# Optimization experiments

Hardware: AMD Instinct MI355X
Metric: run time of the kernel (lower is better)

## Reference

```python
import jax, jax.numpy as jnp
import numpy as np

MIN_DURATION = 0.0
MAX_DURATION = 75.0
MAX_LEN = 80  # hard-coded output length from regulate_length's slice/pad to 80
LN_EPS = 1e-6


def _conv1d_same(x, w, b):
    # x: [B, T, Cin], w: [K, Cin, Cout] -> [B, T, Cout]
    y = jax.lax.conv_general_dilated(
        x, w, window_strides=(1,), padding='SAME',
        dimension_numbers=('NWC', 'WIO', 'NWC'))
    return y + b


def _layernorm(x, gamma, beta):
    mu = jnp.mean(x, axis=-1, keepdims=True)
    var = jnp.mean(jnp.square(x - mu), axis=-1, keepdims=True)
    return (x - mu) * jax.lax.rsqrt(var + LN_EPS) * gamma + beta


def setup_inputs() -> dict:
    key = jax.random.key(0)
    ks = jax.random.split(key, 5)
    B, T, D, F, K = 2048, 128, 256, 256, 3
    scale = 0.05
    return {
        'encoder_output': jax.random.normal(ks[0], (B, T, D), jnp.float32),
        'conv1_w': jax.random.normal(ks[1], (K, D, F), jnp.float32) * scale,
        'conv1_b': jnp.zeros((F,), jnp.float32),
        'conv2_w': jax.random.normal(ks[2], (K, F, F), jnp.float32) * scale,
        'conv2_b': jnp.zeros((F,), jnp.float32),
        'ln_gamma': jnp.ones((F,), jnp.float32),
        'ln_beta': jnp.zeros((F,), jnp.float32),
        'dense_w': jax.random.normal(ks[3], (F, 1), jnp.float32) * scale,
        'dense_b': jnp.full((1,), 2.0, jnp.float32),  # bias so rounded durations are nontrivial
    }


def reference(encoder_output, conv1_w, conv1_b, conv2_w, conv2_b,
              ln_gamma, ln_beta, dense_w, dense_b):
    # --- variance predictor (dropout = identity at inference) ---
    x = jax.nn.relu(_conv1d_same(encoder_output, conv1_w, conv1_b))
    x = _layernorm(x, ln_gamma, ln_beta)
    x = jax.nn.relu(_conv1d_same(x, conv2_w, conv2_b))
    x = _layernorm(x, ln_gamma, ln_beta)
    predicted_durations = x @ dense_w + dense_b  # [B, T, 1]

    # --- regulate_length, fully vectorized over batch ---
    dur = jnp.round(jnp.clip(predicted_durations, MIN_DURATION, MAX_DURATION))
    dur = dur[..., 0].astype(jnp.int32)                 # [B, T]
    cum = jnp.cumsum(dur, axis=1)                       # [B, T]
    pos = jnp.arange(MAX_LEN, dtype=jnp.int32)          # [80]
    # source index for each output frame: searchsorted(cum, pos, side='right')
    idx = jnp.sum(pos[None, :, None] >= cum[:, None, :], axis=-1)  # [B, 80]
    valid = pos[None, :] < cum[:, -1:]                  # [B, 80]
    T = encoder_output.shape[1]
    gathered = jnp.take_along_axis(
        encoder_output, jnp.clip(idx, 0, T - 1)[..., None], axis=1)  # [B, 80, D]
    regulated = jnp.where(valid[..., None], gathered, 0.0)
    return regulated
```

## Files before the change

### kernel.cpp

```cpp
#include <hip/hip_runtime.h>
#include <hip/hip_bf16.h>
#include <math.h>

#define TT 128
#define CC 256
#define MAXLEN 80
#define KSTEPS 24
#define SLOTS 68
#define NCH16 32

typedef __attribute__((ext_vector_type(8))) _Float16 half8v;
typedef __attribute__((ext_vector_type(2))) _Float16 half2v;
typedef __attribute__((ext_vector_type(4))) float f32x4;

#define MSCALE 4096.0f
#define MINV   (1.0f/4096.0f)

__device__ __forceinline__ int chunkidx(int slot, int c16) {
    return slot * NCH16 + (c16 ^ (slot & 7));
}

__device__ __forceinline__ void split2(float x0, float x1, half2v& h, half2v& m) {
    h = __builtin_bit_cast(half2v, __builtin_amdgcn_cvt_pkrtz(x0, x1));
    m.x = (_Float16)fmaf((float)h.x, -MSCALE, x0 * MSCALE);
    m.y = (_Float16)fmaf((float)h.y, -MSCALE, x1 * MSCALE);
}

__global__ void va_prep(const float* __restrict__ w1, const float* __restrict__ w2,
                        half8v* __restrict__ wsB)
{
    const int idx = blockIdx.x * 256 + threadIdx.x;
    const int lane = idx & 63;
    int q = idx >> 6;
    const int nfg = q & 15;   q >>= 4;
    const int plane = q & 1;  q >>= 1;
    const int kk2 = q & 7;    q >>= 3;
    const int tap = q % 3;
    const int cv  = q / 3;
    const float* w = cv ? w2 : w1;
    const int co  = nfg * 16 + (lane & 15);
    const int ci0 = kk2 * 32 + (lane >> 4) * 8;
    half8v out;
    #pragma unroll
    for (int j = 0; j < 8; ++j) {
        const float x = w[tap * (CC * CC) + (ci0 + j) * CC + co];
        const _Float16 h = (_Float16)x;
        if (plane == 0) out[j] = h;
        else            out[j] = (_Float16)((x - (float)h) * MSCALE);
    }
    wsB[idx] = out;
}

__global__ __launch_bounds__(256, 2)
void va_c1(const float* __restrict__ enc,
           const float* __restrict__ b1g,
           const float* __restrict__ gg,  const float* __restrict__ bbg,
           const half8v* __restrict__ wsB,
           half8v* __restrict__ x1G)
{
    __shared__ half8v P[2][SLOTS * NCH16];
    __shared__ float sumS[4][64];
    __shared__ float sumQ[4][64];
    __shared__ float muS[64];
    __shared__ float rsS[64];

    const int bb   = blockIdx.x;
    const int b    = bb >> 1;
    const int base = (bb & 1) << 6;
    const int tid  = threadIdx.x;
    const int wid  = tid >> 6;
    const int lane = tid & 63;
    const int l15  = lane & 15;
    const int lg   = lane >> 4;
    const int NGc  = wid * 64;

    const f32x4* encB4 = reinterpret_cast<const f32x4*>(enc) + (size_t)b * (TT * 64);

    for (int m2 = tid; m2 < SLOTS * NCH16; m2 += 256) {
        const int slot = m2 >> 5;
        const int c16  = m2 & 31;
        const int ra   = base + slot - 2;
        half8v h8, m8;
        if (ra >= 0 && ra < TT) {
            const f32x4* src = encB4 + ra * 64 + c16 * 2;
            const f32x4 v0 = src[0], v1 = src[1];
            half2v hp, mp;
            split2(v0.x, v0.y, hp, mp); h8[0]=hp.x; h8[1]=hp.y; m8[0]=mp.x; m8[1]=mp.y;
            split2(v0.z, v0.w, hp, mp); h8[2]=hp.x; h8[3]=hp.y; m8[2]=mp.x; m8[3]=mp.y;
            split2(v1.x, v1.y, hp, mp); h8[4]=hp.x; h8[5]=hp.y; m8[4]=mp.x; m8[5]=mp.y;
            split2(v1.z, v1.w, hp, mp); h8[6]=hp.x; h8[7]=hp.y; m8[6]=mp.x; m8[7]=mp.y;
        } else {
            #pragma unroll
            for (int j = 0; j < 8; ++j) { h8[j] = (_Float16)0.f; m8[j] = (_Float16)0.f; }
        }
        const int ci = chunkidx(slot, c16);
        P[0][ci] = h8;
        P[1][ci] = m8;
    }
    __syncthreads();

    float gv[4], bvv[4];
    #pragma unroll
    for (int nf = 0; nf < 4; ++nf) {
        gv[nf]  = gg[NGc + nf * 16 + l15];
        bvv[nf] = bbg[NGc + nf * 16 + l15];
    }

    f32x4 accH[4][4];
    f32x4 accM[4][4];
    #pragma unroll
    for (int nf = 0; nf < 4; ++nf) {
        const float bz = b1g[NGc + nf * 16 + l15];
        const f32x4 b4 = {bz, bz, bz, bz};
        const f32x4 z4 = {0.f, 0.f, 0.f, 0.f};
        #pragma unroll
        for (int mf = 0; mf < 4; ++mf) { accH[mf][nf] = b4; accM[mf][nf] = z4; }
    }

    half8v B0[8], B1[8];
    auto loadB = [&](half8v (&Bp)[8], int ks) {
        const int tap = ks >> 3, kk2 = ks & 7;
        const int fb = (tap * 8 + kk2) * 2;
        #pragma unroll
        for (int p = 0; p < 2; ++p)
            #pragma unroll
            for (int nf = 0; nf < 4; ++nf)
                Bp[p * 4 + nf] = wsB[(size_t)((fb + p) * 16 + (wid * 4 + nf)) * 64 + lane];
    };
    auto doK = [&](const half8v (&Bp)[8], int ks) {
        const int tap = ks >> 3, kk2 = ks & 7;
        #pragma unroll
        for (int mf = 0; mf < 4; ++mf) {
            const int slot = mf * 16 + l15 + tap + 1;
            const int ci = chunkidx(slot, kk2 * 4 + lg);
            const half8v Ah = P[0][ci];
            const half8v Am = P[1][ci];
            #pragma unroll
            for (int nf = 0; nf < 4; ++nf) {
                accH[mf][nf] = __builtin_amdgcn_mfma_f32_16x16x32_f16(Ah, Bp[nf],     accH[mf][nf], 0, 0, 0);
                accM[mf][nf] = __builtin_amdgcn_mfma_f32_16x16x32_f16(Ah, Bp[4 + nf], accM[mf][nf], 0, 0, 0);
                accM[mf][nf] = __builtin_amdgcn_mfma_f32_16x16x32_f16(Am, Bp[nf],     accM[mf][nf], 0, 0, 0);
            }
        }
    };
    loadB(B0, 0);
    #pragma unroll 1
    for (int ks = 0; ks < KSTEPS; ks += 2) {
        loadB(B1, ks + 1);
        doK(B0, ks);
        if (ks + 2 < KSTEPS) loadB(B0, ks + 2);
        doK(B1, ks + 1);
    }

    #pragma unroll
    for (int mf = 0; mf < 4; ++mf)
        #pragma unroll
        for (int nf = 0; nf < 4; ++nf) {
            f32x4 v;
            #pragma unroll
            for (int e = 0; e < 4; ++e)
                v[e] = fmaxf(fmaf(accM[mf][nf][e], MINV, accH[mf][nf][e]), 0.f);
            accH[mf][nf] = v;
        }

    #pragma unroll
    for (int mf = 0; mf < 4; ++mf)
        #pragma unroll
        for (int r = 0; r < 4; ++r) {
            float s = (accH[mf][0][r] + accH[mf][1][r]) + (accH[mf][2][r] + accH[mf][3][r]);
            float q = accH[mf][0][r] * accH[mf][0][r];
            q = fmaf(accH[mf][1][r], accH[mf][1][r], q);
            q = fmaf(accH[mf][2][r], accH[mf][2][r], q);
            q = fmaf(accH[mf][3][r], accH[mf][3][r], q);
            #pragma unroll
            for (int o = 1; o < 16; o <<= 1) {
                s += __shfl_xor(s, o, 64);
                q += __shfl_xor(q, o, 64);
            }
            if (l15 == 0) {
                const int idx = mf * 16 + lg * 4 + r;
                sumS[wid][idx] = s;
                sumQ[wid][idx] = q;
            }
        }
    __syncthreads();
    {
        const int i = lane;
        const float S = (sumS[0][i] + sumS[1][i]) + (sumS[2][i] + sumS[3][i]);
        const float Q = (sumQ[0][i] + sumQ[1][i]) + (sumQ[2][i] + sumQ[3][i]);
        const float mu = S * (1.f / 256.f);
        const float var = fmaf(-mu, mu, Q * (1.f / 256.f));
        muS[i] = mu;
        rsS[i] = 1.0f / sqrtf(var + 1e-6f);
    }
    _Float16* Ph = (_Float16*)&P[0][0];
    _Float16* Pm = (_Float16*)&P[1][0];
    #pragma unroll
    for (int mf = 0; mf < 4; ++mf)
        #pragma unroll
        for (int r = 0; r < 4; ++r) {
            const int row = mf * 16 + lg * 4 + r;
            const float mu = muS[row];
            const float rs = rsS[row];
            #pragma unroll
            for (int nf = 0; nf < 4; ++nf) {
                const float v = (accH[mf][nf][r] - mu) * rs * gv[nf] + bvv[nf];
                const int col = NGc + nf * 16 + l15;
                const int off = chunkidx(row + 2, col >> 3) * 8 + (col & 7);
                const _Float16 h = (_Float16)v;
                Ph[off] = h;
                Pm[off] = (_Float16)fmaf((float)h, -MSCALE, v * MSCALE);
            }
        }
    __syncthreads();

    for (int g = tid; g < 2 * 64 * NCH16; g += 256) {
        const int plane = g >> 11;
        const int rem   = g & 2047;
        const int rl    = rem >> 5;
        const int c     = rem & 31;
        x1G[((size_t)(b * 2 + plane) * TT + base + rl) * NCH16 + c] =
            P[plane][(rl + 2) * NCH16 + c];
    }
}

__global__ __launch_bounds__(256, 2)
void va_c2(const half8v* __restrict__ x1G,
           const float* __restrict__ b2g,
           const float* __restrict__ gg,  const float* __restrict__ bbg,
           const float* __restrict__ dwg, const float* __restrict__ dbg,
           const half8v* __restrict__ wsB,
           int* __restrict__ durG)
{
    __shared__ half8v P[2][SLOTS * NCH16];
    __shared__ float sumS[4][64];
    __shared__ float sumQ[4][64];
    __shared__ float muS[64];
    __shared__ float rsS[64];
    __shared__ float dsum[4][64];

    const int bb   = blockIdx.x;
    const int b    = bb >> 1;
    const int base = (bb & 1) << 6;
    const int tid  = threadIdx.x;
    const int wid  = tid >> 6;
    const int lane = tid & 63;
    const int l15  = lane & 15;
    const int lg   = lane >> 4;
    const int NGc  = wid * 64;

    half8v* Plin = &P[0][0];
    for (int g = tid; g < 2 * SLOTS * NCH16; g += 256) {
        const int plane = (g < SLOTS * NCH16) ? 0 : 1;
        const int rem   = g - plane * (SLOTS * NCH16);
        const int slot  = rem >> 5;
        const int c     = rem & 31;
        const int row   = base + slot - 2;
        half8v v;
        if (row >= 0 && row < TT) {
            v = x1G[((size_t)(b * 2 + plane) * TT + row) * NCH16 + c];
        } else {
            #pragma unroll
            for (int j = 0; j < 8; ++j) v[j] = (_Float16)0.f;
        }
        Plin[g] = v;
    }
    __syncthreads();

    float gv[4], bvv[4], dv[4];
    #pragma unroll
    for (int nf = 0; nf < 4; ++nf) {
        gv[nf]  = gg[NGc + nf * 16 + l15];
        bvv[nf] = bbg[NGc + nf * 16 + l15];
        dv[nf]  = dwg[NGc + nf * 16 + l15];
    }

    f32x4 accH[4][4];
    f32x4 accM[4][4];
    #pragma unroll
    for (int nf = 0; nf < 4; ++nf) {
        const float bz = b2g[NGc + nf * 16 + l15];
        const f32x4 b4 = {bz, bz, bz, bz};
        const f32x4 z4 = {0.f, 0.f, 0.f, 0.f};
        #pragma unroll
        for (int mf = 0; mf < 4; ++mf) { accH[mf][nf] = b4; accM[mf][nf] = z4; }
    }

    half8v B0[8], B1[8];
    auto loadB = [&](half8v (&Bp)[8], int ks) {
        const int tap = ks >> 3, kk2 = ks & 7;
        const int fb = ((3 + tap) * 8 + kk2) * 2;
        #pragma unroll
        for (int p = 0; p < 2; ++p)
            #pragma unroll
            for (int nf = 0; nf < 4; ++nf)
                Bp[p * 4 + nf] = wsB[(size_t)((fb + p) * 16 + (wid * 4 + nf)) * 64 + lane];
    };
    auto doK = [&](const half8v (&Bp)[8], int ks) {
        const int tap = ks >> 3, kk2 = ks & 7;
        #pragma unroll
        for (int mf = 0; mf < 4; ++mf) {
            const int slot = mf * 16 + l15 + tap + 1;
            const int ci = chunkidx(slot, kk2 * 4 + lg);
            const half8v Ah = P[0][ci];
            const half8v Am = P[1][ci];
            #pragma unroll
            for (int nf = 0; nf < 4; ++nf) {
                accH[mf][nf] = __builtin_amdgcn_mfma_f32_16x16x32_f16(Ah, Bp[nf],     accH[mf][nf], 0, 0, 0);
                accM[mf][nf] = __builtin_amdgcn_mfma_f32_16x16x32_f16(Ah, Bp[4 + nf], accM[mf][nf], 0, 0, 0);
                accM[mf][nf] = __builtin_amdgcn_mfma_f32_16x16x32_f16(Am, Bp[nf],     accM[mf][nf], 0, 0, 0);
            }
        }
    };
    loadB(B0, 0);
    #pragma unroll 1
    for (int ks = 0; ks < KSTEPS; ks += 2) {
        loadB(B1, ks + 1);
        doK(B0, ks);
        if (ks + 2 < KSTEPS) loadB(B0, ks + 2);
        doK(B1, ks + 1);
    }

    #pragma unroll
    for (int mf = 0; mf < 4; ++mf)
        #pragma unroll
        for (int nf = 0; nf < 4; ++nf) {
            f32x4 v;
            #pragma unroll
            for (int e = 0; e < 4; ++e)
                v[e] = fmaxf(fmaf(accM[mf][nf][e], MINV, accH[mf][nf][e]), 0.f);
            accH[mf][nf] = v;
        }

    #pragma unroll
    for (int mf = 0; mf < 4; ++mf)
        #pragma unroll
        for (int r = 0; r < 4; ++r) {
            float s = (accH[mf][0][r] + accH[mf][1][r]) + (accH[mf][2][r] + accH[mf][3][r]);
            float q = accH[mf][0][r] * accH[mf][0][r];
            q = fmaf(accH[mf][1][r], accH[mf][1][r], q);
            q = fmaf(accH[mf][2][r], accH[mf][2][r], q);
            q = fmaf(accH[mf][3][r], accH[mf][3][r], q);
            #pragma unroll
            for (int o = 1; o < 16; o <<= 1) {
                s += __shfl_xor(s, o, 64);
                q += __shfl_xor(q, o, 64);
            }
            if (l15 == 0) {
                const int idx = mf * 16 + lg * 4 + r;
                sumS[wid][idx] = s;
                sumQ[wid][idx] = q;
            }
        }
    __syncthreads();
    {
        const int i = lane;
        const float S = (sumS[0][i] + sumS[1][i]) + (sumS[2][i] + sumS[3][i]);
        const float Q = (sumQ[0][i] + sumQ[1][i]) + (sumQ[2][i] + sumQ[3][i]);
        const float mu = S * (1.f / 256.f);
        const float var = fmaf(-mu, mu, Q * (1.f / 256.f));
        muS[i] = mu;
        rsS[i] = 1.0f / sqrtf(var + 1e-6f);
    }
    #pragma unroll
    for (int mf = 0; mf < 4; ++mf)
        #pragma unroll
        for (int r = 0; r < 4; ++r) {
            const int row = mf * 16 + lg * 4 + r;
            const float mu = muS[row];
            const float rs = rsS[row];
            float p = 0.f;
            #pragma unroll
            for (int nf = 0; nf < 4; ++nf) {
                const float v = (accH[mf][nf][r] - mu) * rs * gv[nf] + bvv[nf];
                p = fmaf(v, dv[nf], p);
            }
            #pragma unroll
            for (int o = 1; o < 16; o <<= 1) p += __shfl_xor(p, o, 64);
            if (l15 == 0) dsum[wid][row] = p;
        }
    __syncthreads();
    if (tid < 64) {
        const float pd = (dsum[0][tid] + dsum[1][tid]) + (dsum[2][tid] + dsum[3][tid]) + dbg[0];
        const float dcl = fminf(fmaxf(pd, 0.0f), 75.0f);
        durG[b * TT + base + tid] = (int)rintf(dcl);
    }
}

__global__ __launch_bounds__(256)
void va_gather(const float* __restrict__ enc, const int* __restrict__ durG,
               float* __restrict__ outg)
{
    __shared__ int cumS[TT];
    __shared__ int wtotS[2];
    const int b    = blockIdx.x;
    const int tid  = threadIdx.x;
    const int wid  = tid >> 6;
    const int lane = tid & 63;

    int sv = 0;
    if (tid < TT) {
        sv = durG[b * TT + tid];
        #pragma unroll
        for (int o = 1; o < 64; o <<= 1) {
            const int u = __shfl_up(sv, o, 64);
            if (lane >= o) sv += u;
        }
        if (lane == 63) wtotS[tid >> 6] = sv;
    }
    __syncthreads();
    if (tid < TT) {
        if (tid >= 64) sv += wtotS[0];
        cumS[tid] = sv;
    }
    __syncthreads();

    const int total = cumS[TT - 1];
    const f32x4* encB4 = reinterpret_cast<const f32x4*>(enc) + (size_t)b * (TT * 64);
    f32x4* outB4 = reinterpret_cast<f32x4*>(outg) + (size_t)b * (MAXLEN * 64);
    for (int pp = 0; pp < 20; ++pp) {
        const int p = wid * 20 + pp;
        int lo = 0, hi = TT;
        while (lo < hi) {
            const int mid = (lo + hi) >> 1;
            if (cumS[mid] <= p) lo = mid + 1; else hi = mid;
        }
        f32x4 v = {0.f, 0.f, 0.f, 0.f};
        if (p < total) {
            const int src = (lo < TT) ? lo : (TT - 1);
            v = encB4[src * 64 + lane];
        }
        outB4[p * 64 + lane] = v;
    }
}

extern "C" void kernel_launch(void* const* d_in, const int* in_sizes, int n_in,
                              void* d_out, int out_size, void* d_ws, size_t ws_size,
                              hipStream_t stream) {
    const float* enc = (const float*)d_in[0];
    const float* w1  = (const float*)d_in[1];
    const float* b1  = (const float*)d_in[2];
    const float* w2  = (const float*)d_in[3];
    const float* b2  = (const float*)d_in[4];
    const float* gam = (const float*)d_in[5];
    const float* bet = (const float*)d_in[6];
    const float* dw  = (const float*)d_in[7];
    const float* db  = (const float*)d_in[8];
    float* out = (float*)d_out;

    const int B = in_sizes[0] / (TT * CC);
    char* wp = (char*)d_ws;
    half8v* wsB = (half8v*)wp;               wp += 98304u * 16u;
    int* durG   = (int*)wp;                  wp += (size_t)B * TT * 4;
    half8v* x1G = (half8v*)wp;

    const size_t used = (size_t)(wp - (char*)d_ws);
    const size_t perBatch = (size_t)2 * TT * NCH16 * 16;
    size_t avail = (ws_size > used) ? (ws_size - used) : 0;
    int chunkB = (int)(avail / perBatch);
    if (chunkB < 1) chunkB = 1;
    if (chunkB > B) chunkB = B;

    hipLaunchKernelGGL(va_prep, dim3(384), dim3(256), 0, stream, w1, w2, wsB);
    for (int b0 = 0; b0 < B; b0 += chunkB) {
        const int nb = (b0 + chunkB <= B) ? chunkB : (B - b0);
        hipLaunchKernelGGL(va_c1, dim3(nb * 2), dim3(256), 0, stream,
                           enc + (size_t)b0 * TT * CC, b1, gam, bet, wsB, x1G);
        hipLaunchKernelGGL(va_c2, dim3(nb * 2), dim3(256), 0, stream,
                           x1G, b2, gam, bet, dw, db, wsB, durG + (size_t)b0 * TT);
    }
    hipLaunchKernelGGL(va_gather, dim3(B), dim3(256), 0, stream, enc, durG, out);
}
```

Before: 674.3 us.

## Switch conv GEMMs to 32x32x16 MFMA tiles and batch global loads before LDS staging

Both conv kernels now use 32x32x16 f16 MFMA instead of 16x16x32. The prepacked weight layout, accumulator layout, LayerNorm row indexing and shuffle reductions are all rewritten to match. The larger tile is meant to cut LDS A-fragment reads and instruction count per FLOP. Global loads for LDS staging are issued all at once into registers before conversion, to raise memory-level parallelism. Nontemporal loads and stores are added for streaming data. This costs more registers per thread and risks lower occupancy.

```diff
diff --git a/kernel.cpp b/kernel.cpp
--- a/kernel.cpp
+++ b/kernel.cpp
@@ -5,13 +5,14 @@
 #define TT 128
 #define CC 256
 #define MAXLEN 80
-#define KSTEPS 24
+#define KS2 48
 #define SLOTS 68
 #define NCH16 32
 
-typedef __attribute__((ext_vector_type(8))) _Float16 half8v;
-typedef __attribute__((ext_vector_type(2))) _Float16 half2v;
-typedef __attribute__((ext_vector_type(4))) float f32x4;
+typedef __attribute__((ext_vector_type(8)))  _Float16 half8v;
+typedef __attribute__((ext_vector_type(2)))  _Float16 half2v;
+typedef __attribute__((ext_vector_type(4)))  float    f32x4;
+typedef __attribute__((ext_vector_type(16))) float    f32x16;
 
 #define MSCALE 4096.0f
 #define MINV   (1.0f/4096.0f)
@@ -32,14 +33,14 @@
     const int idx = blockIdx.x * 256 + threadIdx.x;
     const int lane = idx & 63;
     int q = idx >> 6;
-    const int nfg = q & 15;   q >>= 4;
+    const int nfg = q & 7;    q >>= 3;
     const int plane = q & 1;  q >>= 1;
-    const int kk2 = q & 7;    q >>= 3;
+    const int kk = q & 15;    q >>= 4;
     const int tap = q % 3;
     const int cv  = q / 3;
     const float* w = cv ? w2 : w1;
-    const int co  = nfg * 16 + (lane & 15);
-    const int ci0 = kk2 * 32 + (lane >> 4) * 8;
+    const int co  = nfg * 32 + (lane & 31);
+    const int ci0 = kk * 16 + (lane >> 5) * 8;
     half8v out;
     #pragma unroll
     for (int j = 0; j < 8; ++j) {
@@ -70,115 +71,126 @@
     const int tid  = threadIdx.x;
     const int wid  = tid >> 6;
     const int lane = tid & 63;
-    const int l15  = lane & 15;
-    const int lg   = lane >> 4;
+    const int l31  = lane & 31;
+    const int hi   = lane >> 5;
     const int NGc  = wid * 64;
 
     const f32x4* encB4 = reinterpret_cast<const f32x4*>(enc) + (size_t)b * (TT * 64);
 
-    for (int m2 = tid; m2 < SLOTS * NCH16; m2 += 256) {
-        const int slot = m2 >> 5;
-        const int c16  = m2 & 31;
-        const int ra   = base + slot - 2;
-        half8v h8, m8;
-        if (ra >= 0 && ra < TT) {
-            const f32x4* src = encB4 + ra * 64 + c16 * 2;
-            const f32x4 v0 = src[0], v1 = src[1];
-            half2v hp, mp;
-            split2(v0.x, v0.y, hp, mp); h8[0]=hp.x; h8[1]=hp.y; m8[0]=mp.x; m8[1]=mp.y;
-            split2(v0.z, v0.w, hp, mp); h8[2]=hp.x; h8[3]=hp.y; m8[2]=mp.x; m8[3]=mp.y;
-            split2(v1.x, v1.y, hp, mp); h8[4]=hp.x; h8[5]=hp.y; m8[4]=mp.x; m8[5]=mp.y;
-            split2(v1.z, v1.w, hp, mp); h8[6]=hp.x; h8[7]=hp.y; m8[6]=mp.x; m8[7]=mp.y;
-        } else {
-            #pragma unroll
-            for (int j = 0; j < 8; ++j) { h8[j] = (_Float16)0.f; m8[j] = (_Float16)0.f; }
-        }
-        const int ci = chunkidx(slot, c16);
-        P[0][ci] = h8;
-        P[1][ci] = m8;
-    }
-    __syncthreads();
-
-    float gv[4], bvv[4];
-    #pragma unroll
-    for (int nf = 0; nf < 4; ++nf) {
-        gv[nf]  = gg[NGc + nf * 16 + l15];
-        bvv[nf] = bbg[NGc + nf * 16 + l15];
-    }
-
-    f32x4 accH[4][4];
-    f32x4 accM[4][4];
-    #pragma unroll
-    for (int nf = 0; nf < 4; ++nf) {
-        const float bz = b1g[NGc + nf * 16 + l15];
-        const f32x4 b4 = {bz, bz, bz, bz};
-        const f32x4 z4 = {0.f, 0.f, 0.f, 0.f};
-        #pragma unroll
-        for (int mf = 0; mf < 4; ++mf) { accH[mf][nf] = b4; accM[mf][nf] = z4; }
-    }
-
-    half8v B0[8], B1[8];
-    auto loadB = [&](half8v (&Bp)[8], int ks) {
-        const int tap = ks >> 3, kk2 = ks & 7;
-        const int fb = (tap * 8 + kk2) * 2;
+    {
+        f32x4 sa[9], sb[9];
+        #pragma unroll
+        for (int it = 0; it < 9; ++it) {
+            const f32x4 z = {0.f, 0.f, 0.f, 0.f};
+            sa[it] = z; sb[it] = z;
+            const int m2 = tid + it * 256;
+            if (m2 < SLOTS * NCH16) {
+                const int slot = m2 >> 5;
+                const int c16  = m2 & 31;
+                const int ra   = base + slot - 2;
+                if (ra >= 0 && ra < TT) {
+                    const f32x4* src = encB4 + ra * 64 + c16 * 2;
+                    sa[it] = __builtin_nontemporal_load(src);
+                    sb[it] = __builtin_nontemporal_load(src + 1);
+                }
+            }
+        }
+        #pragma unroll
+        for (int it = 0; it < 9; ++it) {
+            const int m2 = tid + it * 256;
+            if (m2 < SLOTS * NCH16) {
+                const f32x4 v0 = sa[it], v1 = sb[it];
+                half8v h8, m8;
+                half2v hp, mp;
+                split2(v0.x, v0.y, hp, mp); h8[0]=hp.x; h8[1]=hp.y; m8[0]=mp.x; m8[1]=mp.y;
+                split2(v0.z, v0.w, hp, mp); h8[2]=hp.x; h8[3]=hp.y; m8[2]=mp.x; m8[3]=mp.y;
+                split2(v1.x, v1.y, hp, mp); h8[4]=hp.x; h8[5]=hp.y; m8[4]=mp.x; m8[5]=mp.y;
+                split2(v1.z, v1.w, hp, mp); h8[6]=hp.x; h8[7]=hp.y; m8[6]=mp.x; m8[7]=mp.y;
+                const int ci = chunkidx(m2 >> 5, m2 & 31);
+                P[0][ci] = h8;
+                P[1][ci] = m8;
+            }
+        }
+    }
+    __syncthreads();
+
+    float gv[2], bvv[2];
+    #pragma unroll
+    for (int nf = 0; nf < 2; ++nf) {
+        gv[nf]  = gg[NGc + nf * 32 + l31];
+        bvv[nf] = bbg[NGc + nf * 32 + l31];
+    }
+
+    f32x16 accH[2][2];
+    f32x16 accM[2][2];
+    #pragma unroll
+    for (int nf = 0; nf < 2; ++nf) {
+        const float bz = b1g[NGc + nf * 32 + l31];
+        #pragma unroll
+        for (int mf = 0; mf < 2; ++mf)
+            #pragma unroll
+            for (int e = 0; e < 16; ++e) { accH[mf][nf][e] = bz; accM[mf][nf][e] = 0.f; }
+    }
+
+    half8v B0[4], B1[4];
+    auto loadB = [&](half8v (&Bp)[4], int ks) {
+        const int tap = ks >> 4, kk = ks & 15;
+        const int fb = ((0 * 3 + tap) * 16 + kk) * 2;
         #pragma unroll
         for (int p = 0; p < 2; ++p)
             #pragma unroll
-            for (int nf = 0; nf < 4; ++nf)
-                Bp[p * 4 + nf] = wsB[(size_t)((fb + p) * 16 + (wid * 4 + nf)) * 64 + lane];
+            for (int nf = 0; nf < 2; ++nf)
+                Bp[p * 2 + nf] = wsB[(size_t)((fb + p) * 8 + (wid * 2 + nf)) * 64 + lane];
     };
-    auto doK = [&](const half8v (&Bp)[8], int ks) {
-        const int tap = ks >> 3, kk2 = ks & 7;
-        #pragma unroll
-        for (int mf = 0; mf < 4; ++mf) {
-            const int slot = mf * 16 + l15 + tap + 1;
-            const int ci = chunkidx(slot, kk2 * 4 + lg);
+    auto doK = [&](const half8v (&Bp)[4], int ks) {
+        const int tap = ks >> 4, kk = ks & 15;
+        #pragma unroll
+        for (int mf = 0; mf < 2; ++mf) {
+            const int slot = mf * 32 + l31 + tap + 1;
+            const int ci = chunkidx(slot, kk * 2 + hi);
             const half8v Ah = P[0][ci];
             const half8v Am = P[1][ci];
             #pragma unroll
-            for (int nf = 0; nf < 4; ++nf) {
-                accH[mf][nf] = __builtin_amdgcn_mfma_f32_16x16x32_f16(Ah, Bp[nf],     accH[mf][nf], 0, 0, 0);
-                accM[mf][nf] = __builtin_amdgcn_mfma_f32_16x16x32_f16(Ah, Bp[4 + nf], accM[mf][nf], 0, 0, 0);
-                accM[mf][nf] = __builtin_amdgcn_mfma_f32_16x16x32_f16(Am, Bp[nf],     accM[mf][nf], 0, 0, 0);
-            }
+            for (int nf = 0; nf < 2; ++nf)
+                accH[mf][nf] = __builtin_amdgcn_mfma_f32_32x32x16_f16(Ah, Bp[nf],     accH[mf][nf], 0, 0, 0);
+            #pragma unroll
+            for (int nf = 0; nf < 2; ++nf)
+                accM[mf][nf] = __builtin_amdgcn_mfma_f32_32x32x16_f16(Ah, Bp[2 + nf], accM[mf][nf], 0, 0, 0);
+            #pragma unroll
+            for (int nf = 0; nf < 2; ++nf)
+                accM[mf][nf] = __builtin_amdgcn_mfma_f32_32x32x16_f16(Am, Bp[nf],     accM[mf][nf], 0, 0, 0);
         }
     };
     loadB(B0, 0);
     #pragma unroll 1
-    for (int ks = 0; ks < KSTEPS; ks += 2) {
+    for (int ks = 0; ks < KS2; ks += 2) {
         loadB(B1, ks + 1);
         doK(B0, ks);
-        if (ks + 2 < KSTEPS) loadB(B0, ks + 2);
+        if (ks + 2 < KS2) loadB(B0, ks + 2);
         doK(B1, ks + 1);
     }
 
     #pragma unroll
-    for (int mf = 0; mf < 4; ++mf)
-        #pragma unroll
-        for (int nf = 0; nf < 4; ++nf) {
-            f32x4 v;
-            #pragma unroll
-            for (int e = 0; e < 4; ++e)
-                v[e] = fmaxf(fmaf(accM[mf][nf][e], MINV, accH[mf][nf][e]), 0.f);
-            accH[mf][nf] = v;
-        }
-
-    #pragma unroll
-    for (int mf = 0; mf < 4; ++mf)
-        #pragma unroll
-        for (int r = 0; r < 4; ++r) {
-            float s = (accH[mf][0][r] + accH[mf][1][r]) + (accH[mf][2][r] + accH[mf][3][r]);
-            float q = accH[mf][0][r] * accH[mf][0][r];
-            q = fmaf(accH[mf][1][r], accH[mf][1][r], q);
-            q = fmaf(accH[mf][2][r], accH[mf][2][r], q);
-            q = fmaf(accH[mf][3][r], accH[mf][3][r], q);
-            #pragma unroll
-            for (int o = 1; o < 16; o <<= 1) {
+    for (int mf = 0; mf < 2; ++mf)
+        #pragma unroll
+        for (int nf = 0; nf < 2; ++nf)
+            #pragma unroll
+            for (int e = 0; e < 16; ++e)
+                accH[mf][nf][e] = fmaxf(fmaf(accM[mf][nf][e], MINV, accH[mf][nf][e]), 0.f);
+
+    #pragma unroll
+    for (int mf = 0; mf < 2; ++mf)
+        #pragma unroll
+        for (int r = 0; r < 16; ++r) {
+            float s = accH[mf][0][r] + accH[mf][1][r];
+            float q = fmaf(accH[mf][0][r], accH[mf][0][r], accH[mf][1][r] * accH[mf][1][r]);
+            #pragma unroll
+            for (int o = 1; o < 32; o <<= 1) {
                 s += __shfl_xor(s, o, 64);
                 q += __shfl_xor(q, o, 64);
             }
-            if (l15 == 0) {
-                const int idx = mf * 16 + lg * 4 + r;
+            if (l31 == 0) {
+                const int idx = mf * 32 + (r & 3) + 8 * (r >> 2) + 4 * hi;
                 sumS[wid][idx] = s;
                 sumQ[wid][idx] = q;
             }
@@ -196,16 +208,16 @@
     _Float16* Ph = (_Float16*)&P[0][0];
     _Float16* Pm = (_Float16*)&P[1][0];
     #pragma unroll
-    for (int mf = 0; mf < 4; ++mf)
-        #pragma unroll
-        for (int r = 0; r < 4; ++r) {
-            const int row = mf * 16 + lg * 4 + r;
+    for (int mf = 0; mf < 2; ++mf)
+        #pragma unroll
+        for (int r = 0; r < 16; ++r) {
+            const int row = mf * 32 + (r & 3) + 8 * (r >> 2) + 4 * hi;
             const float mu = muS[row];
             const float rs = rsS[row];
             #pragma unroll
-            for (int nf = 0; nf < 4; ++nf) {
+            for (int nf = 0; nf < 2; ++nf) {
                 const float v = (accH[mf][nf][r] - mu) * rs * gv[nf] + bvv[nf];
-                const int col = NGc + nf * 16 + l15;
+                const int col = NGc + nf * 32 + l31;
                 const int off = chunkidx(row + 2, col >> 3) * 8 + (col & 7);
                 const _Float16 h = (_Float16)v;
                 Ph[off] = h;
@@ -245,109 +257,112 @@
     const int tid  = threadIdx.x;
     const int wid  = tid >> 6;
     const int lane = tid & 63;
-    const int l15  = lane & 15;
-    const int lg   = lane >> 4;
+    const int l31  = lane & 31;
+    const int hi   = lane >> 5;
     const int NGc  = wid * 64;
 
-    half8v* Plin = &P[0][0];
-    for (int g = tid; g < 2 * SLOTS * NCH16; g += 256) {
-        const int plane = (g < SLOTS * NCH16) ? 0 : 1;
-        const int rem   = g - plane * (SLOTS * NCH16);
-        const int slot  = rem >> 5;
-        const int c     = rem & 31;
-        const int row   = base + slot - 2;
-        half8v v;
-        if (row >= 0 && row < TT) {
-            v = x1G[((size_t)(b * 2 + plane) * TT + row) * NCH16 + c];
-        } else {
-            #pragma unroll
-            for (int j = 0; j < 8; ++j) v[j] = (_Float16)0.f;
-        }
-        Plin[g] = v;
-    }
-    __syncthreads();
-
-    float gv[4], bvv[4], dv[4];
-    #pragma unroll
-    for (int nf = 0; nf < 4; ++nf) {
-        gv[nf]  = gg[NGc + nf * 16 + l15];
-        bvv[nf] = bbg[NGc + nf * 16 + l15];
-        dv[nf]  = dwg[NGc + nf * 16 + l15];
-    }
-
-    f32x4 accH[4][4];
-    f32x4 accM[4][4];
-    #pragma unroll
-    for (int nf = 0; nf < 4; ++nf) {
-        const float bz = b2g[NGc + nf * 16 + l15];
-        const f32x4 b4 = {bz, bz, bz, bz};
-        const f32x4 z4 = {0.f, 0.f, 0.f, 0.f};
-        #pragma unroll
-        for (int mf = 0; mf < 4; ++mf) { accH[mf][nf] = b4; accM[mf][nf] = z4; }
-    }
-
-    half8v B0[8], B1[8];
-    auto loadB = [&](half8v (&Bp)[8], int ks) {
-        const int tap = ks >> 3, kk2 = ks & 7;
-        const int fb = ((3 + tap) * 8 + kk2) * 2;
+    {
+        half8v sx[17];
+        #pragma unroll
+        for (int it = 0; it < 17; ++it) {
+            const int g = tid + it * 256;
+            const int plane = (g >= SLOTS * NCH16) ? 1 : 0;
+            const int rem   = g - plane * (SLOTS * NCH16);
+            const int slot  = rem >> 5;
+            const int c     = rem & 31;
+            const int row   = base + slot - 2;
+            if (row >= 0 && row < TT) {
+                sx[it] = x1G[((size_t)(b * 2 + plane) * TT + row) * NCH16 + c];
+            } else {
+                #pragma unroll
+                for (int j = 0; j < 8; ++j) sx[it][j] = (_Float16)0.f;
+            }
+        }
+        half8v* Plin = &P[0][0];
+        #pragma unroll
+        for (int it = 0; it < 17; ++it)
+            Plin[tid + it * 256] = sx[it];
+    }
+    __syncthreads();
+
+    float gv[2], bvv[2], dv[2];
+    #pragma unroll
+    for (int nf = 0; nf < 2; ++nf) {
+        gv[nf]  = gg[NGc + nf * 32 + l31];
+        bvv[nf] = bbg[NGc + nf * 32 + l31];
+        dv[nf]  = dwg[NGc + nf * 32 + l31];
+    }
+
+    f32x16 accH[2][2];
+    f32x16 accM[2][2];
+    #pragma unroll
+    for (int nf = 0; nf < 2; ++nf) {
+        const float bz = b2g[NGc + nf * 32 + l31];
+        #pragma unroll
+        for (int mf = 0; mf < 2; ++mf)
+            #pragma unroll
+            for (int e = 0; e < 16; ++e) { accH[mf][nf][e] = bz; accM[mf][nf][e] = 0.f; }
+    }
+
+    half8v B0[4], B1[4];
+    auto loadB = [&](half8v (&Bp)[4], int ks) {
+        const int tap = ks >> 4, kk = ks & 15;
+        const int fb = ((1 * 3 + tap) * 16 + kk) * 2;
         #pragma unroll
         for (int p = 0; p < 2; ++p)
             #pragma unroll
-            for (int nf = 0; nf < 4; ++nf)
-                Bp[p * 4 + nf] = wsB[(size_t)((fb + p) * 16 + (wid * 4 + nf)) * 64 + lane];
+            for (int nf = 0; nf < 2; ++nf)
+                Bp[p * 2 + nf] = wsB[(size_t)((fb + p) * 8 + (wid * 2 + nf)) * 64 + lane];
     };
-    auto doK = [&](const half8v (&Bp)[8], int ks) {
-        const int tap = ks >> 3, kk2 = ks & 7;
-        #pragma unroll
-        for (int mf = 0; mf < 4; ++mf) {
-            const int slot = mf * 16 + l15 + tap + 1;
-            const int ci = chunkidx(slot, kk2 * 4 + lg);
+    auto doK = [&](const half8v (&Bp)[4], int ks) {
+        const int tap = ks >> 4, kk = ks & 15;
+        #pragma unroll
+        for (int mf = 0; mf < 2; ++mf) {
+            const int slot = mf * 32 + l31 + tap + 1;
+            const int ci = chunkidx(slot, kk * 2 + hi);
             const half8v Ah = P[0][ci];
             const half8v Am = P[1][ci];
             #pragma unroll
-            for (int nf = 0; nf < 4; ++nf) {
-                accH[mf][nf] = __builtin_amdgcn_mfma_f32_16x16x32_f16(Ah, Bp[nf],     accH[mf][nf], 0, 0, 0);
-                accM[mf][nf] = __builtin_amdgcn_mfma_f32_16x16x32_f16(Ah, Bp[4 + nf], accM[mf][nf], 0, 0, 0);
-                accM[mf][nf] = __builtin_amdgcn_mfma_f32_16x16x32_f16(Am, Bp[nf],     accM[mf][nf], 0, 0, 0);
-            }
+            for (int nf = 0; nf < 2; ++nf)
+                accH[mf][nf] = __builtin_amdgcn_mfma_f32_32x32x16_f16(Ah, Bp[nf],     accH[mf][nf], 0, 0, 0);
+            #pragma unroll
+            for (int nf = 0; nf < 2; ++nf)
+                accM[mf][nf] = __builtin_amdgcn_mfma_f32_32x32x16_f16(Ah, Bp[2 + nf], accM[mf][nf], 0, 0, 0);
+            #pragma unroll
+            for (int nf = 0; nf < 2; ++nf)
+                accM[mf][nf] = __builtin_amdgcn_mfma_f32_32x32x16_f16(Am, Bp[nf],     accM[mf][nf], 0, 0, 0);
         }
     };
     loadB(B0, 0);
     #pragma unroll 1
-    for (int ks = 0; ks < KSTEPS; ks += 2) {
+    for (int ks = 0; ks < KS2; ks += 2) {
         loadB(B1, ks + 1);
         doK(B0, ks);
-        if (ks + 2 < KSTEPS) loadB(B0, ks + 2);
+        if (ks + 2 < KS2) loadB(B0, ks + 2);
         doK(B1, ks + 1);
     }
 
     #pragma unroll
-    for (int mf = 0; mf < 4; ++mf)
-        #pragma unroll
-        for (int nf = 0; nf < 4; ++nf) {
-            f32x4 v;
-            #pragma unroll
-            for (int e = 0; e < 4; ++e)
-                v[e] = fmaxf(fmaf(accM[mf][nf][e], MINV, accH[mf][nf][e]), 0.f);
-            accH[mf][nf] = v;
-        }
-
-    #pragma unroll
-    for (int mf = 0; mf < 4; ++mf)
-        #pragma unroll
-        for (int r = 0; r < 4; ++r) {
-            float s = (accH[mf][0][r] + accH[mf][1][r]) + (accH[mf][2][r] + accH[mf][3][r]);
-            float q = accH[mf][0][r] * accH[mf][0][r];
-            q = fmaf(accH[mf][1][r], accH[mf][1][r], q);
-            q = fmaf(accH[mf][2][r], accH[mf][2][r], q);
-            q = fmaf(accH[mf][3][r], accH[mf][3][r], q);
-            #pragma unroll
-            for (int o = 1; o < 16; o <<= 1) {
+    for (int mf = 0; mf < 2; ++mf)
+        #pragma unroll
+        for (int nf = 0; nf < 2; ++nf)
+            #pragma unroll
+            for (int e = 0; e < 16; ++e)
+                accH[mf][nf][e] = fmaxf(fmaf(accM[mf][nf][e], MINV, accH[mf][nf][e]), 0.f);
+
+    #pragma unroll
+    for (int mf = 0; mf < 2; ++mf)
+        #pragma unroll
+        for (int r = 0; r < 16; ++r) {
+            float s = accH[mf][0][r] + accH[mf][1][r];
+            float q = fmaf(accH[mf][0][r], accH[mf][0][r], accH[mf][1][r] * accH[mf][1][r]);
+            #pragma unroll
+            for (int o = 1; o < 32; o <<= 1) {
                 s += __shfl_xor(s, o, 64);
                 q += __shfl_xor(q, o, 64);
             }
-            if (l15 == 0) {
-                const int idx = mf * 16 + lg * 4 + r;
+            if (l31 == 0) {
+                const int idx = mf * 32 + (r & 3) + 8 * (r >> 2) + 4 * hi;
                 sumS[wid][idx] = s;
                 sumQ[wid][idx] = q;
             }
@@ -363,21 +378,21 @@
         rsS[i] = 1.0f / sqrtf(var + 1e-6f);
     }
     #pragma unroll
-    for (int mf = 0; mf < 4; ++mf)
-        #pragma unroll
-        for (int r = 0; r < 4; ++r) {
-            const int row = mf * 16 + lg * 4 + r;
+    for (int mf = 0; mf < 2; ++mf)
+        #pragma unroll
+        for (int r = 0; r < 16; ++r) {
+            const int row = mf * 32 + (r & 3) + 8 * (r >> 2) + 4 * hi;
             const float mu = muS[row];
             const float rs = rsS[row];
             float p = 0.f;
             #pragma unroll
-            for (int nf = 0; nf < 4; ++nf) {
+            for (int nf = 0; nf < 2; ++nf) {
                 const float v = (accH[mf][nf][r] - mu) * rs * gv[nf] + bvv[nf];
                 p = fmaf(v, dv[nf], p);
             }
             #pragma unroll
-            for (int o = 1; o < 16; o <<= 1) p += __shfl_xor(p, o, 64);
-            if (l15 == 0) dsum[wid][row] = p;
+            for (int o = 1; o < 32; o <<= 1) p += __shfl_xor(p, o, 64);
+            if (l31 == 0) dsum[wid][row] = p;
         }
     __syncthreads();
     if (tid < 64) {
@@ -420,17 +435,17 @@
     f32x4* outB4 = reinterpret_cast<f32x4*>(outg) + (size_t)b * (MAXLEN * 64);
     for (int pp = 0; pp < 20; ++pp) {
         const int p = wid * 20 + pp;
-        int lo = 0, hi = TT;
-        while (lo < hi) {
-            const int mid = (lo + hi) >> 1;
-            if (cumS[mid] <= p) lo = mid + 1; else hi = mid;
+        int lo = 0, hi2 = TT;
+        while (lo < hi2) {
+            const int mid = (lo + hi2) >> 1;
+            if (cumS[mid] <= p) lo = mid + 1; else hi2 = mid;
         }
         f32x4 v = {0.f, 0.f, 0.f, 0.f};
         if (p < total) {
             const int src = (lo < TT) ? lo : (TT - 1);
-            v = encB4[src * 64 + lane];
-        }
-        outB4[p * 64 + lane] = v;
+            v = __builtin_nontemporal_load(&encB4[src * 64 + lane]);
+        }
+        __builtin_nontemporal_store(v, &outB4[p * 64 + lane]);
     }
 }
 
```

After: 801.6 us. 18.9% more time.
